# Kernel tuning notes

Measured on AMD Instinct MI355X. Metric: run time of the kernel, lower is better.

The kernel has to match this reference:

```python
import jax, jax.numpy as jnp
import numpy as np

B, T, S, H = 8, 128, 256, 512


def setup_inputs() -> dict:
    key = jax.random.key(0)
    ks = jax.random.split(key, 8)
    query = jax.random.normal(ks[0], (B, T, H), dtype=jnp.float32)
    encoder_outputs = jax.random.normal(ks[1], (B, S, H), dtype=jnp.float32)
    # lengths in [S//2, S], with max pinned to S (torch code requires lengths.max() == mask width == S)
    src_lengths = jax.random.randint(ks[2], (B,), S // 2, S + 1)
    src_lengths = src_lengths.at[0].set(S)
    scale = 1.0 / np.sqrt(H)
    W_s = jax.random.normal(ks[3], (H, H), dtype=jnp.float32) * scale
    W_h = jax.random.normal(ks[4], (H, H), dtype=jnp.float32) * scale
    v = jax.random.normal(ks[5], (H,), dtype=jnp.float32) * scale
    W_out = jax.random.normal(ks[6], (H, 2 * H), dtype=jnp.float32) * (1.0 / np.sqrt(2 * H))
    b_out = jax.random.normal(ks[7], (H,), dtype=jnp.float32) * 0.01
    return {"query": query, "encoder_outputs": encoder_outputs, "src_lengths": src_lengths,
            "W_s": W_s, "W_h": W_h, "v": v, "W_out": W_out, "b_out": b_out}


def reference(query, encoder_outputs, src_lengths, W_s, W_h, v, W_out, b_out):
    # Projections (torch Linear: x @ W.T)
    qs = jnp.einsum('bth,kh->btk', query, W_s)            # (B,T,H)
    hs = jnp.einsum('bsh,kh->bsk', encoder_outputs, W_h)  # (B,S,H)
    # Additive score: v . tanh(W_s q + W_h h) -> (B,T,S)
    scores = jnp.einsum('btsh,h->bts', jnp.tanh(qs[:, :, None, :] + hs[:, None, :, :]), v)
    mask = jnp.arange(scores.shape[-1])[None, :] < src_lengths[:, None]  # (B,S)
    scores = jnp.where(mask[:, None, :], scores, -jnp.inf)
    attn = jax.nn.softmax(scores, axis=-1)                # (B,T,S)
    context = jnp.einsum('bts,bsh->bth', attn, encoder_outputs)
    combined = jnp.concatenate([context, query], axis=-1)  # (B,T,2H)
    return jnp.tanh(jnp.einsum('btc,hc->bth', combined, W_out) + b_out)
```

## Files before the change

kernel.cpp:

```cpp
#include <hip/hip_runtime.h>

constexpr int B = 8, T = 128, S = 256, H = 512;

typedef __attribute__((ext_vector_type(4))) float f32x4;
typedef __attribute__((ext_vector_type(8))) float f32x8;
typedef __attribute__((ext_vector_type(8))) short short8;
typedef __attribute__((ext_vector_type(4))) short short4v;

#define DEVINL __device__ __forceinline__

DEVINL float bf2f(short s) {
  union { unsigned u; float f; } x;
  x.u = ((unsigned)(unsigned short)s) << 16;
  return x.f;
}
DEVINL short f2bf(float f) {
  unsigned u = __float_as_uint(f);
  return (short)((u + 0x7fffu + ((u >> 16) & 1u)) >> 16);
}
DEVINL float fast_tanh(float x) {
  float e = __builtin_amdgcn_exp2f(x * 2.8853900817779268f);
  return 1.0f - 2.0f * __builtin_amdgcn_rcpf(e + 1.0f);
}

constexpr float C2 = 2.8853900817779268f;
constexpr float L2E = 1.4426950408889634f;

constexpr size_t OFF_EH  = 0;
constexpr size_t OFF_PT  = OFF_EH + (size_t)B * H * S;
constexpr size_t OFF_ATT = OFF_PT + (size_t)B * H * S;
constexpr size_t OFF_QBF = OFF_ATT + (size_t)B * T * S;
constexpr size_t OFF_EBF = OFF_QBF + (size_t)B * T * H;
constexpr size_t OFF_WSB = OFF_EBF + (size_t)B * S * H;
constexpr size_t OFF_WHB = OFF_WSB + (size_t)H * H;
constexpr size_t OFF_WOB = OFF_WHB + (size_t)H * H;
constexpr size_t OFF_EQ  = OFF_WOB + (size_t)H * 2 * H;

__global__ __launch_bounds__(256) void prep_kernel(
    const float* __restrict__ q, const float* __restrict__ e,
    const float* __restrict__ ws, const float* __restrict__ wh,
    const float* __restrict__ wo, short* __restrict__ base) {
  int vi = blockIdx.x * 256 + threadIdx.x;
  if (vi >= 655360) return;
  const float* src; short* dst; int local; float scale;
  if (vi < 131072)      { src = q;  dst = base + OFF_QBF; local = vi;          scale = 1.f; }
  else if (vi < 393216) { src = e;  dst = base + OFF_EBF; local = vi - 131072; scale = 1.f; }
  else if (vi < 458752) { src = ws; dst = base + OFF_WSB; local = vi - 393216; scale = C2;  }
  else if (vi < 524288) { src = wh; dst = base + OFF_WHB; local = vi - 458752; scale = C2;  }
  else                  { src = wo; dst = base + OFF_WOB; local = vi - 524288; scale = 1.f; }
  float4 f = reinterpret_cast<const float4*>(src)[local];
  short4v o;
  o.x = f2bf(f.x * scale); o.y = f2bf(f.y * scale);
  o.z = f2bf(f.z * scale); o.w = f2bf(f.w * scale);
  *reinterpret_cast<short4v*>(dst + (size_t)local * 4) = o;
}

template <int MB>
DEVINL void gemm_tile_bf(const short* __restrict__ A, int lda,
                         const short* __restrict__ Wt, int ldw, int K,
                         int bm, int bn, short* As, short* Bs, f32x4* acc) {
  const int tid = threadIdx.x;
  const int lane = tid & 63;
  const int wm = (tid >> 6) >> 1, wn = (tid >> 6) & 1;
  const int g = lane >> 4, r = lane & 15;
  for (int k0 = 0; k0 < K; k0 += 64) {
    __syncthreads();
#pragma unroll
    for (int p = 0; p < MB; ++p) {
      const int idx = p * 256 + tid;
      const int row = idx >> 3, c = idx & 7;
      short8 av = *reinterpret_cast<const short8*>(&A[(size_t)(bm + row) * lda + k0 + c * 8]);
      *reinterpret_cast<short8*>(&As[row * 64 + ((c ^ (row & 7)) * 8)]) = av;
    }
#pragma unroll
    for (int p = 0; p < 2; ++p) {
      const int idx = p * 256 + tid;
      const int row = idx >> 3, c = idx & 7;
      short8 wv = *reinterpret_cast<const short8*>(&Wt[(size_t)(bn + row) * ldw + k0 + c * 8]);
      *reinterpret_cast<short8*>(&Bs[row * 64 + ((c ^ (row & 7)) * 8)]) = wv;
    }
    __syncthreads();
#pragma unroll
    for (int kc = 0; kc < 2; ++kc) {
      short8 af[MB], bfr[2];
#pragma unroll
      for (int mb = 0; mb < MB; ++mb) {
        const int ra = wm * (MB * 16) + mb * 16 + r;
        af[mb] = *reinterpret_cast<const short8*>(&As[ra * 64 + (((kc * 4 + g) ^ (r & 7)) * 8)]);
      }
#pragma unroll
      for (int nb = 0; nb < 2; ++nb) {
        const int rb = wn * 32 + nb * 16 + r;
        bfr[nb] = *reinterpret_cast<const short8*>(&Bs[rb * 64 + (((kc * 4 + g) ^ (r & 7)) * 8)]);
      }
#pragma unroll
      for (int mb = 0; mb < MB; ++mb)
#pragma unroll
        for (int nb = 0; nb < 2; ++nb)
          acc[mb * 2 + nb] =
              __builtin_amdgcn_mfma_f32_16x16x32_bf16(af[mb], bfr[nb], acc[mb * 2 + nb], 0, 0, 0);
    }
  }
}

__global__ __launch_bounds__(256) void proj_kernel(short* __restrict__ wsbase,
                                                   float* __restrict__ eq) {
  __shared__ short As[64 * 64], Bs[64 * 64];
  f32x4 acc[4];
#pragma unroll
  for (int i = 0; i < 4; ++i) acc[i] = (f32x4){0.f, 0.f, 0.f, 0.f};
  int bid = blockIdx.x;
  int mode; const short* A; const short* W; int ldw;
  const short* q_bf = wsbase + OFF_QBF;
  const short* e_bf = wsbase + OFF_EBF;
  if (bid < 128)      { mode = 0; A = q_bf; W = wsbase + OFF_WSB; ldw = H; }
  else if (bid < 384) { mode = 1; bid -= 128; A = e_bf; W = wsbase + OFF_WHB; ldw = H; }
  else                { mode = 2; bid -= 384; A = e_bf; W = wsbase + OFF_WOB; ldw = 2 * H; }
  const int bm = (bid >> 3) * 64, bn = (bid & 7) * 64;
  gemm_tile_bf<2>(A, H, W, ldw, H, bm, bn, As, Bs, acc);

  short* eh_p = wsbase + OFF_EH;
  short* P_t = wsbase + OFF_PT;
  const int lane = threadIdx.x & 63, wave = threadIdx.x >> 6;
  const int wm = wave >> 1, wn = wave & 1, g = lane >> 4, r = lane & 15;
#pragma unroll
  for (int mb = 0; mb < 2; ++mb)
#pragma unroll
    for (int nb = 0; nb < 2; ++nb) {
      const f32x4 a4 = acc[mb * 2 + nb];
      const int m0 = bm + wm * 32 + mb * 16 + g * 4;
      const int col = bn + wn * 32 + nb * 16 + r;
      if (mode == 0) {
#pragma unroll
        for (int i = 0; i < 4; ++i)
          eq[(size_t)(m0 + i) * H + col] = __builtin_amdgcn_exp2f(a4[i]);
      } else if (mode == 1) {
        const int bb = m0 >> 8, sl = m0 & 255;
        const size_t base = ((size_t)(bb * (H / 8) + (col >> 3)) * S + sl) * 8 + (col & 7);
#pragma unroll
        for (int i = 0; i < 4; ++i)
          eh_p[base + (size_t)i * 8] = f2bf(__builtin_amdgcn_exp2f(a4[i]));
      } else {
        const int bb = m0 >> 8, sl = m0 & 255;
        short4v o;
        o.x = f2bf(a4[0]); o.y = f2bf(a4[1]); o.z = f2bf(a4[2]); o.w = f2bf(a4[3]);
        *reinterpret_cast<short4v*>(&P_t[((size_t)bb * H + col) * S + sl]) = o;
      }
    }
}

__global__ __launch_bounds__(512) void attn_kernel(
    const float* __restrict__ eq, const short* __restrict__ eh_p,
    const float* __restrict__ v, const int* __restrict__ lens,
    short* __restrict__ attn_bf) {
  __shared__ float s_part[2][2][S];
  __shared__ float red_m[2][4], red_s[2][4];
  const int tid = threadIdx.x, lane = tid & 63;
  const int wu = __builtin_amdgcn_readfirstlane(tid >> 6);
  const int sg = wu & 3, half = wu >> 2;
  const int b = blockIdx.x >> 6;
  const int t0 = (blockIdx.x & 63) * 2;
  const int s = sg * 64 + lane;

  const float* qp0 = eq + (size_t)(b * T + t0) * H + half * (H / 2);
  const float* qp1 = qp0 + H;
  const float* vp = v + half * (H / 2);
  const short8* ep = reinterpret_cast<const short8*>(eh_p) +
                     ((size_t)(b * (H / 8) + half * (H / 16)) * S + s);

  float acc0 = 0.f, acc1 = 0.f;
  short8 e0 = ep[0], e1 = ep[(size_t)S];
  f32x8 qA0 = *reinterpret_cast<const f32x8*>(qp0);
  f32x8 qB0 = *reinterpret_cast<const f32x8*>(qp0 + 8);
  f32x8 qA1 = *reinterpret_cast<const f32x8*>(qp1);
  f32x8 qB1 = *reinterpret_cast<const f32x8*>(qp1 + 8);
  f32x8 vA = *reinterpret_cast<const f32x8*>(vp);
  f32x8 vB = *reinterpret_cast<const f32x8*>(vp + 8);
  for (int it = 0; it < 16; ++it) {
    const int nh = (it < 15) ? (it + 1) * 16 : 0;
    const size_t ne = (it < 15) ? (size_t)(2 * it + 2) * S : 0;
    const short8 e0n = ep[ne], e1n = ep[ne + S];
    const f32x8 qA0n = *reinterpret_cast<const f32x8*>(qp0 + nh);
    const f32x8 qB0n = *reinterpret_cast<const f32x8*>(qp0 + nh + 8);
    const f32x8 qA1n = *reinterpret_cast<const f32x8*>(qp1 + nh);
    const f32x8 qB1n = *reinterpret_cast<const f32x8*>(qp1 + nh + 8);
    const f32x8 vAn = *reinterpret_cast<const f32x8*>(vp + nh);
    const f32x8 vBn = *reinterpret_cast<const f32x8*>(vp + nh + 8);
#pragma unroll
    for (int j = 0; j < 8; ++j) {
      const float e = bf2f(e0[j]);
      acc0 = fmaf(vA[j], __builtin_amdgcn_rcpf(fmaf(qA0[j], e, 1.0f)), acc0);
      acc1 = fmaf(vA[j], __builtin_amdgcn_rcpf(fmaf(qA1[j], e, 1.0f)), acc1);
    }
#pragma unroll
    for (int j = 0; j < 8; ++j) {
      const float e = bf2f(e1[j]);
      acc0 = fmaf(vB[j], __builtin_amdgcn_rcpf(fmaf(qB0[j], e, 1.0f)), acc0);
      acc1 = fmaf(vB[j], __builtin_amdgcn_rcpf(fmaf(qB1[j], e, 1.0f)), acc1);
    }
    e0 = e0n; e1 = e1n;
    qA0 = qA0n; qB0 = qB0n; qA1 = qA1n; qB1 = qB1n;
    vA = vAn; vB = vBn;
  }
  s_part[half][0][s] = acc0;
  s_part[half][1][s] = acc1;
  __syncthreads();

  const int len = lens[b];
  const float a0 = s_part[0][0][s] + s_part[1][0][s];
  const float a1 = s_part[0][1][s] + s_part[1][1][s];
  const float y0 = (s < len) ? (-2.0f * L2E * a0) : -1e30f;
  const float y1 = (s < len) ? (-2.0f * L2E * a1) : -1e30f;
  float m0 = y0, m1 = y1;
#pragma unroll
  for (int off = 32; off > 0; off >>= 1) {
    m0 = fmaxf(m0, __shfl_xor(m0, off));
    m1 = fmaxf(m1, __shfl_xor(m1, off));
  }
  if (lane == 0) { red_m[0][sg] = m0; red_m[1][sg] = m1; }
  __syncthreads();
  const float mt0 = fmaxf(fmaxf(red_m[0][0], red_m[0][1]), fmaxf(red_m[0][2], red_m[0][3]));
  const float mt1 = fmaxf(fmaxf(red_m[1][0], red_m[1][1]), fmaxf(red_m[1][2], red_m[1][3]));
  const float p0 = __builtin_amdgcn_exp2f(y0 - mt0);
  const float p1 = __builtin_amdgcn_exp2f(y1 - mt1);
  float u0 = p0, u1 = p1;
#pragma unroll
  for (int off = 32; off > 0; off >>= 1) {
    u0 += __shfl_xor(u0, off);
    u1 += __shfl_xor(u1, off);
  }
  if (lane == 0) { red_s[0][sg] = u0; red_s[1][sg] = u1; }
  __syncthreads();
  if (half == 0) {
    const float tot0 = red_s[0][0] + red_s[0][1] + red_s[0][2] + red_s[0][3];
    const float tot1 = red_s[1][0] + red_s[1][1] + red_s[1][2] + red_s[1][3];
    attn_bf[(size_t)(b * T + t0) * S + s] = f2bf(p0 * __builtin_amdgcn_rcpf(tot0));
    attn_bf[(size_t)(b * T + t0 + 1) * S + s] = f2bf(p1 * __builtin_amdgcn_rcpf(tot1));
  }
}

__global__ __launch_bounds__(256) void out_kernel(
    const short* __restrict__ wsbase, const float* __restrict__ bias,
    float* __restrict__ out) {
  __shared__ short As[32 * 64], Bs[64 * 64];
  f32x4 acc[2];
#pragma unroll
  for (int i = 0; i < 2; ++i) acc[i] = (f32x4){0.f, 0.f, 0.f, 0.f};
  const int bm = (blockIdx.x >> 3) * 32, bn = (blockIdx.x & 7) * 64;
  const int batch = bm >> 7;
  const short* attn_bf = wsbase + OFF_ATT;
  const short* P_t = wsbase + OFF_PT;
  const short* q_bf = wsbase + OFF_QBF;
  const short* Wob = wsbase + OFF_WOB;
  gemm_tile_bf<1>(attn_bf, S, P_t + (size_t)batch * H * S, S, S, bm, bn, As, Bs, acc);
  gemm_tile_bf<1>(q_bf, H, Wob + H, 2 * H, H, bm, bn, As, Bs, acc);
  const int lane = threadIdx.x & 63, wave = threadIdx.x >> 6;
  const int wm = wave >> 1, wn = wave & 1, g = lane >> 4, r = lane & 15;
#pragma unroll
  for (int nb = 0; nb < 2; ++nb) {
    const f32x4 a4 = acc[nb];
    const int col = bn + wn * 32 + nb * 16 + r;
    const float bb = bias[col];
#pragma unroll
    for (int i = 0; i < 4; ++i) {
      const int row = bm + wm * 16 + g * 4 + i;
      out[(size_t)row * H + col] = fast_tanh(a4[i] + bb);
    }
  }
}

extern "C" void kernel_launch(void* const* d_in, const int* in_sizes, int n_in,
                              void* d_out, int out_size, void* d_ws, size_t ws_size,
                              hipStream_t stream) {
  const float* query = (const float*)d_in[0];
  const float* enc = (const float*)d_in[1];
  const int* lens = (const int*)d_in[2];
  const float* W_s = (const float*)d_in[3];
  const float* W_h = (const float*)d_in[4];
  const float* v = (const float*)d_in[5];
  const float* W_out = (const float*)d_in[6];
  const float* b_out = (const float*)d_in[7];
  float* out = (float*)d_out;

  short* wsb = (short*)d_ws;
  short* eh_p = wsb + OFF_EH;
  short* attn_bf = wsb + OFF_ATT;
  float* eq = (float*)(wsb + OFF_EQ);

  prep_kernel<<<2560, 256, 0, stream>>>(query, enc, W_s, W_h, W_out, wsb);
  proj_kernel<<<640, 256, 0, stream>>>(wsb, eq);
  attn_kernel<<<B * T / 2, 512, 0, stream>>>(eq, eh_p, v, lens, attn_bf);
  out_kernel<<<256, 256, 0, stream>>>(wsb, b_out, out);
}
```

Baseline: 48.85 us.

## Pair reciprocals in attention score loop and widen GEMM N-tiles to 128

The attention inner loop now combines two terms v_j/A + v_{j+1}/B into a single (v_j*B + v_{j+1}*A)/(A*B), halving the number of transcendental rcp instructions per element at the cost of a few extra multiplies and some overflow risk when A*B is large. Separately, the projection and output GEMMs double their N tile from 64 to 128, giving each wave 4 MFMA column blocks. This halves the grid sizes (640→320, 256→128) and improves operand reuse from shared memory, but on a large GPU it lowers the block count and the occupancy of each CU.

```diff
diff --git a/kernel.cpp b/kernel.cpp
--- a/kernel.cpp
+++ b/kernel.cpp
@@ -55,7 +55,7 @@
   *reinterpret_cast<short4v*>(dst + (size_t)local * 4) = o;
 }
 
-template <int MB>
+template <int MB, int NB>
 DEVINL void gemm_tile_bf(const short* __restrict__ A, int lda,
                          const short* __restrict__ Wt, int ldw, int K,
                          int bm, int bn, short* As, short* Bs, f32x4* acc) {
@@ -73,7 +73,7 @@
       *reinterpret_cast<short8*>(&As[row * 64 + ((c ^ (row & 7)) * 8)]) = av;
     }
 #pragma unroll
-    for (int p = 0; p < 2; ++p) {
+    for (int p = 0; p < NB; ++p) {
       const int idx = p * 256 + tid;
       const int row = idx >> 3, c = idx & 7;
       short8 wv = *reinterpret_cast<const short8*>(&Wt[(size_t)(bn + row) * ldw + k0 + c * 8]);
@@ -82,42 +82,42 @@
     __syncthreads();
 #pragma unroll
     for (int kc = 0; kc < 2; ++kc) {
-      short8 af[MB], bfr[2];
+      short8 af[MB], bfr[NB];
 #pragma unroll
       for (int mb = 0; mb < MB; ++mb) {
         const int ra = wm * (MB * 16) + mb * 16 + r;
         af[mb] = *reinterpret_cast<const short8*>(&As[ra * 64 + (((kc * 4 + g) ^ (r & 7)) * 8)]);
       }
 #pragma unroll
-      for (int nb = 0; nb < 2; ++nb) {
-        const int rb = wn * 32 + nb * 16 + r;
+      for (int nb = 0; nb < NB; ++nb) {
+        const int rb = wn * (NB * 16) + nb * 16 + r;
         bfr[nb] = *reinterpret_cast<const short8*>(&Bs[rb * 64 + (((kc * 4 + g) ^ (r & 7)) * 8)]);
       }
 #pragma unroll
       for (int mb = 0; mb < MB; ++mb)
 #pragma unroll
-        for (int nb = 0; nb < 2; ++nb)
-          acc[mb * 2 + nb] =
-              __builtin_amdgcn_mfma_f32_16x16x32_bf16(af[mb], bfr[nb], acc[mb * 2 + nb], 0, 0, 0);
+        for (int nb = 0; nb < NB; ++nb)
+          acc[mb * NB + nb] =
+              __builtin_amdgcn_mfma_f32_16x16x32_bf16(af[mb], bfr[nb], acc[mb * NB + nb], 0, 0, 0);
     }
   }
 }
 
 __global__ __launch_bounds__(256) void proj_kernel(short* __restrict__ wsbase,
                                                    float* __restrict__ eq) {
-  __shared__ short As[64 * 64], Bs[64 * 64];
-  f32x4 acc[4];
-#pragma unroll
-  for (int i = 0; i < 4; ++i) acc[i] = (f32x4){0.f, 0.f, 0.f, 0.f};
+  __shared__ short As[64 * 64], Bs[128 * 64];
+  f32x4 acc[8];
+#pragma unroll
+  for (int i = 0; i < 8; ++i) acc[i] = (f32x4){0.f, 0.f, 0.f, 0.f};
   int bid = blockIdx.x;
   int mode; const short* A; const short* W; int ldw;
   const short* q_bf = wsbase + OFF_QBF;
   const short* e_bf = wsbase + OFF_EBF;
-  if (bid < 128)      { mode = 0; A = q_bf; W = wsbase + OFF_WSB; ldw = H; }
-  else if (bid < 384) { mode = 1; bid -= 128; A = e_bf; W = wsbase + OFF_WHB; ldw = H; }
-  else                { mode = 2; bid -= 384; A = e_bf; W = wsbase + OFF_WOB; ldw = 2 * H; }
-  const int bm = (bid >> 3) * 64, bn = (bid & 7) * 64;
-  gemm_tile_bf<2>(A, H, W, ldw, H, bm, bn, As, Bs, acc);
+  if (bid < 64)       { mode = 0; A = q_bf; W = wsbase + OFF_WSB; ldw = H; }
+  else if (bid < 192) { mode = 1; bid -= 64; A = e_bf; W = wsbase + OFF_WHB; ldw = H; }
+  else                { mode = 2; bid -= 192; A = e_bf; W = wsbase + OFF_WOB; ldw = 2 * H; }
+  const int bm = (bid >> 2) * 64, bn = (bid & 3) * 128;
+  gemm_tile_bf<2, 4>(A, H, W, ldw, H, bm, bn, As, Bs, acc);
 
   short* eh_p = wsbase + OFF_EH;
   short* P_t = wsbase + OFF_PT;
@@ -126,10 +126,10 @@
 #pragma unroll
   for (int mb = 0; mb < 2; ++mb)
 #pragma unroll
-    for (int nb = 0; nb < 2; ++nb) {
-      const f32x4 a4 = acc[mb * 2 + nb];
+    for (int nb = 0; nb < 4; ++nb) {
+      const f32x4 a4 = acc[mb * 4 + nb];
       const int m0 = bm + wm * 32 + mb * 16 + g * 4;
-      const int col = bn + wn * 32 + nb * 16 + r;
+      const int col = bn + wn * 64 + nb * 16 + r;
       if (mode == 0) {
 #pragma unroll
         for (int i = 0; i < 4; ++i)
@@ -187,16 +187,40 @@
     const f32x8 vAn = *reinterpret_cast<const f32x8*>(vp + nh);
     const f32x8 vBn = *reinterpret_cast<const f32x8*>(vp + nh + 8);
 #pragma unroll
-    for (int j = 0; j < 8; ++j) {
-      const float e = bf2f(e0[j]);
-      acc0 = fmaf(vA[j], __builtin_amdgcn_rcpf(fmaf(qA0[j], e, 1.0f)), acc0);
-      acc1 = fmaf(vA[j], __builtin_amdgcn_rcpf(fmaf(qA1[j], e, 1.0f)), acc1);
-    }
-#pragma unroll
-    for (int j = 0; j < 8; ++j) {
-      const float e = bf2f(e1[j]);
-      acc0 = fmaf(vB[j], __builtin_amdgcn_rcpf(fmaf(qB0[j], e, 1.0f)), acc0);
-      acc1 = fmaf(vB[j], __builtin_amdgcn_rcpf(fmaf(qB1[j], e, 1.0f)), acc1);
+    for (int j = 0; j < 8; j += 2) {
+      const float ea = bf2f(e0[j]), eb = bf2f(e0[j + 1]);
+      {
+        const float Aa = fmaf(qA0[j], ea, 1.0f);
+        const float Bb = fmaf(qA0[j + 1], eb, 1.0f);
+        const float rr = __builtin_amdgcn_rcpf(Aa * Bb);
+        const float num = fmaf(vA[j + 1], Aa, vA[j] * Bb);
+        acc0 = fmaf(num, rr, acc0);
+      }
+      {
+        const float Aa = fmaf(qA1[j], ea, 1.0f);
+        const float Bb = fmaf(qA1[j + 1], eb, 1.0f);
+        const float rr = __builtin_amdgcn_rcpf(Aa * Bb);
+        const float num = fmaf(vA[j + 1], Aa, vA[j] * Bb);
+        acc1 = fmaf(num, rr, acc1);
+      }
+    }
+#pragma unroll
+    for (int j = 0; j < 8; j += 2) {
+      const float ea = bf2f(e1[j]), eb = bf2f(e1[j + 1]);
+      {
+        const float Aa = fmaf(qB0[j], ea, 1.0f);
+        const float Bb = fmaf(qB0[j + 1], eb, 1.0f);
+        const float rr = __builtin_amdgcn_rcpf(Aa * Bb);
+        const float num = fmaf(vB[j + 1], Aa, vB[j] * Bb);
+        acc0 = fmaf(num, rr, acc0);
+      }
+      {
+        const float Aa = fmaf(qB1[j], ea, 1.0f);
+        const float Bb = fmaf(qB1[j + 1], eb, 1.0f);
+        const float rr = __builtin_amdgcn_rcpf(Aa * Bb);
+        const float num = fmaf(vB[j + 1], Aa, vB[j] * Bb);
+        acc1 = fmaf(num, rr, acc1);
+      }
     }
     e0 = e0n; e1 = e1n;
     qA0 = qA0n; qB0 = qB0n; qA1 = qA1n; qB1 = qB1n;
@@ -242,24 +266,24 @@
 __global__ __launch_bounds__(256) void out_kernel(
     const short* __restrict__ wsbase, const float* __restrict__ bias,
     float* __restrict__ out) {
-  __shared__ short As[32 * 64], Bs[64 * 64];
-  f32x4 acc[2];
-#pragma unroll
-  for (int i = 0; i < 2; ++i) acc[i] = (f32x4){0.f, 0.f, 0.f, 0.f};
-  const int bm = (blockIdx.x >> 3) * 32, bn = (blockIdx.x & 7) * 64;
+  __shared__ short As[32 * 64], Bs[128 * 64];
+  f32x4 acc[4];
+#pragma unroll
+  for (int i = 0; i < 4; ++i) acc[i] = (f32x4){0.f, 0.f, 0.f, 0.f};
+  const int bm = (blockIdx.x >> 2) * 32, bn = (blockIdx.x & 3) * 128;
   const int batch = bm >> 7;
   const short* attn_bf = wsbase + OFF_ATT;
   const short* P_t = wsbase + OFF_PT;
   const short* q_bf = wsbase + OFF_QBF;
   const short* Wob = wsbase + OFF_WOB;
-  gemm_tile_bf<1>(attn_bf, S, P_t + (size_t)batch * H * S, S, S, bm, bn, As, Bs, acc);
-  gemm_tile_bf<1>(q_bf, H, Wob + H, 2 * H, H, bm, bn, As, Bs, acc);
+  gemm_tile_bf<1, 4>(attn_bf, S, P_t + (size_t)batch * H * S, S, S, bm, bn, As, Bs, acc);
+  gemm_tile_bf<1, 4>(q_bf, H, Wob + H, 2 * H, H, bm, bn, As, Bs, acc);
   const int lane = threadIdx.x & 63, wave = threadIdx.x >> 6;
   const int wm = wave >> 1, wn = wave & 1, g = lane >> 4, r = lane & 15;
 #pragma unroll
-  for (int nb = 0; nb < 2; ++nb) {
+  for (int nb = 0; nb < 4; ++nb) {
     const f32x4 a4 = acc[nb];
-    const int col = bn + wn * 32 + nb * 16 + r;
+    const int col = bn + wn * 64 + nb * 16 + r;
     const float bb = bias[col];
 #pragma unroll
     for (int i = 0; i < 4; ++i) {
@@ -288,7 +312,7 @@
   float* eq = (float*)(wsb + OFF_EQ);
 
   prep_kernel<<<2560, 256, 0, stream>>>(query, enc, W_s, W_h, W_out, wsb);
-  proj_kernel<<<640, 256, 0, stream>>>(wsb, eq);
+  proj_kernel<<<320, 256, 0, stream>>>(wsb, eq);
   attn_kernel<<<B * T / 2, 512, 0, stream>>>(eq, eh_p, v, lens, attn_bf);
-  out_kernel<<<256, 256, 0, stream>>>(wsb, b_out, out);
-}
+  out_kernel<<<128, 256, 0, stream>>>(wsb, b_out, out);
+}
```

Result: slower. 50.54 us (+3.5%).

## Pair reciprocals in attention scores and process four queries per block

Applied to the files above, without the earlier changes.

The attention kernel now computes four query rows per 1024-thread block, splitting H into quarters, so each loaded encoder value is reused across four queries. It also merges two reciprocals into one by computing vA/A + vB/B as (vB*A + vA*B)/(A*B), which halves the rcp instructions in the inner loop. The GEMM helper gains an NB template parameter, but the existing call sites keep the same shape. Risks include overflow or precision loss in the A*B product, reduced occupancy with 1024-thread blocks, and less latency hiding because the q/v prefetch was removed.

```diff
diff --git a/kernel.cpp b/kernel.cpp
--- a/kernel.cpp
+++ b/kernel.cpp
@@ -55,7 +55,7 @@
   *reinterpret_cast<short4v*>(dst + (size_t)local * 4) = o;
 }
 
-template <int MB>
+template <int MB, int NB>
 DEVINL void gemm_tile_bf(const short* __restrict__ A, int lda,
                          const short* __restrict__ Wt, int ldw, int K,
                          int bm, int bn, short* As, short* Bs, f32x4* acc) {
@@ -73,7 +73,7 @@
       *reinterpret_cast<short8*>(&As[row * 64 + ((c ^ (row & 7)) * 8)]) = av;
     }
 #pragma unroll
-    for (int p = 0; p < 2; ++p) {
+    for (int p = 0; p < NB; ++p) {
       const int idx = p * 256 + tid;
       const int row = idx >> 3, c = idx & 7;
       short8 wv = *reinterpret_cast<const short8*>(&Wt[(size_t)(bn + row) * ldw + k0 + c * 8]);
@@ -82,23 +82,23 @@
     __syncthreads();
 #pragma unroll
     for (int kc = 0; kc < 2; ++kc) {
-      short8 af[MB], bfr[2];
+      short8 af[MB], bfr[NB];
 #pragma unroll
       for (int mb = 0; mb < MB; ++mb) {
         const int ra = wm * (MB * 16) + mb * 16 + r;
         af[mb] = *reinterpret_cast<const short8*>(&As[ra * 64 + (((kc * 4 + g) ^ (r & 7)) * 8)]);
       }
 #pragma unroll
-      for (int nb = 0; nb < 2; ++nb) {
-        const int rb = wn * 32 + nb * 16 + r;
+      for (int nb = 0; nb < NB; ++nb) {
+        const int rb = wn * (NB * 16) + nb * 16 + r;
         bfr[nb] = *reinterpret_cast<const short8*>(&Bs[rb * 64 + (((kc * 4 + g) ^ (r & 7)) * 8)]);
       }
 #pragma unroll
       for (int mb = 0; mb < MB; ++mb)
 #pragma unroll
-        for (int nb = 0; nb < 2; ++nb)
-          acc[mb * 2 + nb] =
-              __builtin_amdgcn_mfma_f32_16x16x32_bf16(af[mb], bfr[nb], acc[mb * 2 + nb], 0, 0, 0);
+        for (int nb = 0; nb < NB; ++nb)
+          acc[mb * NB + nb] =
+              __builtin_amdgcn_mfma_f32_16x16x32_bf16(af[mb], bfr[nb], acc[mb * NB + nb], 0, 0, 0);
     }
   }
 }
@@ -117,7 +117,7 @@
   else if (bid < 384) { mode = 1; bid -= 128; A = e_bf; W = wsbase + OFF_WHB; ldw = H; }
   else                { mode = 2; bid -= 384; A = e_bf; W = wsbase + OFF_WOB; ldw = 2 * H; }
   const int bm = (bid >> 3) * 64, bn = (bid & 7) * 64;
-  gemm_tile_bf<2>(A, H, W, ldw, H, bm, bn, As, Bs, acc);
+  gemm_tile_bf<2, 2>(A, H, W, ldw, H, bm, bn, As, Bs, acc);
 
   short* eh_p = wsbase + OFF_EH;
   short* P_t = wsbase + OFF_PT;
@@ -149,93 +149,97 @@
     }
 }
 
-__global__ __launch_bounds__(512) void attn_kernel(
+__global__ __launch_bounds__(1024) void attn_kernel(
     const float* __restrict__ eq, const short* __restrict__ eh_p,
     const float* __restrict__ v, const int* __restrict__ lens,
     short* __restrict__ attn_bf) {
-  __shared__ float s_part[2][2][S];
-  __shared__ float red_m[2][4], red_s[2][4];
+  __shared__ float s_part[4][4][S];
+  __shared__ float red_m[4][4], red_s[4][4];
   const int tid = threadIdx.x, lane = tid & 63;
   const int wu = __builtin_amdgcn_readfirstlane(tid >> 6);
-  const int sg = wu & 3, half = wu >> 2;
-  const int b = blockIdx.x >> 6;
-  const int t0 = (blockIdx.x & 63) * 2;
+  const int sg = wu & 3, qtr = wu >> 2;
+  const int b = blockIdx.x >> 5;
+  const int t0 = (blockIdx.x & 31) * 4;
   const int s = sg * 64 + lane;
 
-  const float* qp0 = eq + (size_t)(b * T + t0) * H + half * (H / 2);
-  const float* qp1 = qp0 + H;
-  const float* vp = v + half * (H / 2);
+  const float* qp = eq + (size_t)(b * T + t0) * H + qtr * (H / 4);
+  const float* vp = v + qtr * (H / 4);
   const short8* ep = reinterpret_cast<const short8*>(eh_p) +
-                     ((size_t)(b * (H / 8) + half * (H / 16)) * S + s);
-
-  float acc0 = 0.f, acc1 = 0.f;
+                     ((size_t)(b * (H / 8) + qtr * (H / 32)) * S + s);
+
+  float acc[4] = {0.f, 0.f, 0.f, 0.f};
   short8 e0 = ep[0], e1 = ep[(size_t)S];
-  f32x8 qA0 = *reinterpret_cast<const f32x8*>(qp0);
-  f32x8 qB0 = *reinterpret_cast<const f32x8*>(qp0 + 8);
-  f32x8 qA1 = *reinterpret_cast<const f32x8*>(qp1);
-  f32x8 qB1 = *reinterpret_cast<const f32x8*>(qp1 + 8);
-  f32x8 vA = *reinterpret_cast<const f32x8*>(vp);
-  f32x8 vB = *reinterpret_cast<const f32x8*>(vp + 8);
-  for (int it = 0; it < 16; ++it) {
-    const int nh = (it < 15) ? (it + 1) * 16 : 0;
-    const size_t ne = (it < 15) ? (size_t)(2 * it + 2) * S : 0;
+  for (int it = 0; it < 8; ++it) {
+    const size_t ne = (it < 7) ? (size_t)(2 * it + 2) * S : 0;
     const short8 e0n = ep[ne], e1n = ep[ne + S];
-    const f32x8 qA0n = *reinterpret_cast<const f32x8*>(qp0 + nh);
-    const f32x8 qB0n = *reinterpret_cast<const f32x8*>(qp0 + nh + 8);
-    const f32x8 qA1n = *reinterpret_cast<const f32x8*>(qp1 + nh);
-    const f32x8 qB1n = *reinterpret_cast<const f32x8*>(qp1 + nh + 8);
-    const f32x8 vAn = *reinterpret_cast<const f32x8*>(vp + nh);
-    const f32x8 vBn = *reinterpret_cast<const f32x8*>(vp + nh + 8);
-#pragma unroll
-    for (int j = 0; j < 8; ++j) {
-      const float e = bf2f(e0[j]);
-      acc0 = fmaf(vA[j], __builtin_amdgcn_rcpf(fmaf(qA0[j], e, 1.0f)), acc0);
-      acc1 = fmaf(vA[j], __builtin_amdgcn_rcpf(fmaf(qA1[j], e, 1.0f)), acc1);
-    }
-#pragma unroll
-    for (int j = 0; j < 8; ++j) {
-      const float e = bf2f(e1[j]);
-      acc0 = fmaf(vB[j], __builtin_amdgcn_rcpf(fmaf(qB0[j], e, 1.0f)), acc0);
-      acc1 = fmaf(vB[j], __builtin_amdgcn_rcpf(fmaf(qB1[j], e, 1.0f)), acc1);
+    const int h = it * 16;
+    float ef[16];
+#pragma unroll
+    for (int j = 0; j < 8; ++j) { ef[j] = bf2f(e0[j]); ef[8 + j] = bf2f(e1[j]); }
+    const f32x8 vA = *reinterpret_cast<const f32x8*>(vp + h);
+    const f32x8 vB = *reinterpret_cast<const f32x8*>(vp + h + 8);
+#pragma unroll
+    for (int tt = 0; tt < 4; ++tt) {
+      const float* qq = qp + (size_t)tt * H + h;
+      const f32x8 qA = *reinterpret_cast<const f32x8*>(qq);
+      const f32x8 qB = *reinterpret_cast<const f32x8*>(qq + 8);
+#pragma unroll
+      for (int j = 0; j < 8; j += 2) {
+        const float Aa = fmaf(qA[j], ef[j], 1.0f);
+        const float Bb = fmaf(qA[j + 1], ef[j + 1], 1.0f);
+        const float rr = __builtin_amdgcn_rcpf(Aa * Bb);
+        acc[tt] = fmaf(fmaf(vA[j + 1], Aa, vA[j] * Bb), rr, acc[tt]);
+      }
+#pragma unroll
+      for (int j = 0; j < 8; j += 2) {
+        const float Aa = fmaf(qB[j], ef[8 + j], 1.0f);
+        const float Bb = fmaf(qB[j + 1], ef[8 + j + 1], 1.0f);
+        const float rr = __builtin_amdgcn_rcpf(Aa * Bb);
+        acc[tt] = fmaf(fmaf(vB[j + 1], Aa, vB[j] * Bb), rr, acc[tt]);
+      }
     }
     e0 = e0n; e1 = e1n;
-    qA0 = qA0n; qB0 = qB0n; qA1 = qA1n; qB1 = qB1n;
-    vA = vAn; vB = vBn;
-  }
-  s_part[half][0][s] = acc0;
-  s_part[half][1][s] = acc1;
+  }
+#pragma unroll
+  for (int tt = 0; tt < 4; ++tt) s_part[qtr][tt][s] = acc[tt];
   __syncthreads();
 
   const int len = lens[b];
-  const float a0 = s_part[0][0][s] + s_part[1][0][s];
-  const float a1 = s_part[0][1][s] + s_part[1][1][s];
-  const float y0 = (s < len) ? (-2.0f * L2E * a0) : -1e30f;
-  const float y1 = (s < len) ? (-2.0f * L2E * a1) : -1e30f;
-  float m0 = y0, m1 = y1;
-#pragma unroll
-  for (int off = 32; off > 0; off >>= 1) {
-    m0 = fmaxf(m0, __shfl_xor(m0, off));
-    m1 = fmaxf(m1, __shfl_xor(m1, off));
-  }
-  if (lane == 0) { red_m[0][sg] = m0; red_m[1][sg] = m1; }
+  float y[4], m[4];
+#pragma unroll
+  for (int tt = 0; tt < 4; ++tt) {
+    const float a = s_part[0][tt][s] + s_part[1][tt][s] + s_part[2][tt][s] + s_part[3][tt][s];
+    y[tt] = (s < len) ? (-2.0f * L2E * a) : -1e30f;
+    m[tt] = y[tt];
+#pragma unroll
+    for (int off = 32; off > 0; off >>= 1) m[tt] = fmaxf(m[tt], __shfl_xor(m[tt], off));
+  }
+  if (qtr == 0 && lane == 0) {
+#pragma unroll
+    for (int tt = 0; tt < 4; ++tt) red_m[tt][sg] = m[tt];
+  }
   __syncthreads();
-  const float mt0 = fmaxf(fmaxf(red_m[0][0], red_m[0][1]), fmaxf(red_m[0][2], red_m[0][3]));
-  const float mt1 = fmaxf(fmaxf(red_m[1][0], red_m[1][1]), fmaxf(red_m[1][2], red_m[1][3]));
-  const float p0 = __builtin_amdgcn_exp2f(y0 - mt0);
-  const float p1 = __builtin_amdgcn_exp2f(y1 - mt1);
-  float u0 = p0, u1 = p1;
-#pragma unroll
-  for (int off = 32; off > 0; off >>= 1) {
-    u0 += __shfl_xor(u0, off);
-    u1 += __shfl_xor(u1, off);
-  }
-  if (lane == 0) { red_s[0][sg] = u0; red_s[1][sg] = u1; }
+  float p[4], u[4];
+#pragma unroll
+  for (int tt = 0; tt < 4; ++tt) {
+    const float mt = fmaxf(fmaxf(red_m[tt][0], red_m[tt][1]),
+                           fmaxf(red_m[tt][2], red_m[tt][3]));
+    p[tt] = __builtin_amdgcn_exp2f(y[tt] - mt);
+    u[tt] = p[tt];
+#pragma unroll
+    for (int off = 32; off > 0; off >>= 1) u[tt] += __shfl_xor(u[tt], off);
+  }
+  if (qtr == 0 && lane == 0) {
+#pragma unroll
+    for (int tt = 0; tt < 4; ++tt) red_s[tt][sg] = u[tt];
+  }
   __syncthreads();
-  if (half == 0) {
-    const float tot0 = red_s[0][0] + red_s[0][1] + red_s[0][2] + red_s[0][3];
-    const float tot1 = red_s[1][0] + red_s[1][1] + red_s[1][2] + red_s[1][3];
-    attn_bf[(size_t)(b * T + t0) * S + s] = f2bf(p0 * __builtin_amdgcn_rcpf(tot0));
-    attn_bf[(size_t)(b * T + t0 + 1) * S + s] = f2bf(p1 * __builtin_amdgcn_rcpf(tot1));
+  if (qtr == 0) {
+#pragma unroll
+    for (int tt = 0; tt < 4; ++tt) {
+      const float tot = red_s[tt][0] + red_s[tt][1] + red_s[tt][2] + red_s[tt][3];
+      attn_bf[(size_t)(b * T + t0 + tt) * S + s] = f2bf(p[tt] * __builtin_amdgcn_rcpf(tot));
+    }
   }
 }
 
@@ -252,8 +256,8 @@
   const short* P_t = wsbase + OFF_PT;
   const short* q_bf = wsbase + OFF_QBF;
   const short* Wob = wsbase + OFF_WOB;
-  gemm_tile_bf<1>(attn_bf, S, P_t + (size_t)batch * H * S, S, S, bm, bn, As, Bs, acc);
-  gemm_tile_bf<1>(q_bf, H, Wob + H, 2 * H, H, bm, bn, As, Bs, acc);
+  gemm_tile_bf<1, 2>(attn_bf, S, P_t + (size_t)batch * H * S, S, S, bm, bn, As, Bs, acc);
+  gemm_tile_bf<1, 2>(q_bf, H, Wob + H, 2 * H, H, bm, bn, As, Bs, acc);
   const int lane = threadIdx.x & 63, wave = threadIdx.x >> 6;
   const int wm = wave >> 1, wn = wave & 1, g = lane >> 4, r = lane & 15;
 #pragma unroll
@@ -289,6 +293,6 @@
 
   prep_kernel<<<2560, 256, 0, stream>>>(query, enc, W_s, W_h, W_out, wsb);
   proj_kernel<<<640, 256, 0, stream>>>(wsb, eq);
-  attn_kernel<<<B * T / 2, 512, 0, stream>>>(eq, eh_p, v, lens, attn_bf);
+  attn_kernel<<<B * T / 4, 1024, 0, stream>>>(eq, eh_p, v, lens, attn_bf);
   out_kernel<<<256, 256, 0, stream>>>(wsb, b_out, out);
 }
```

New measurement: 47.82 us. 1.02x faster.
